# Optimization experiments

Hardware: AMD Instinct MI355X
Metric: run time of the kernel (lower is better)

## Reference

```python
import jax, jax.numpy as jnp
import numpy as np
from itertools import combinations

BASIS = 16  # identity + sums over every nonempty subset of the 4 set axes


def eq4_layer(x, coefs, bias):
    """Permutation-equivariant 4->4 set layer.
    x: (B, Din, n, n, n, n); coefs: (Din, Dout, 16); bias: (Dout,)
    Basis op 0 is identity; ops 1..15 are sums over each nonempty subset of the
    four set axes, broadcast back to full shape. We never stack the 16 full-size
    ops: pooled ops are contracted in their small (keepdims) form and broadcast-added.
    """
    out = jnp.einsum('ds,bdijkl->bsijkl', coefs[:, :, 0], x)
    b = 1
    for r in range(1, 5):
        for axes in combinations((2, 3, 4, 5), r):
            m = x.sum(axis=axes, keepdims=True)  # small marginal tensor
            out = out + jnp.einsum('ds,bd...->bs...', coefs[:, :, b], m)
            b += 1
    return out + bias.reshape(1, -1, 1, 1, 1, 1)


def setup_inputs() -> dict:
    key = jax.random.key(0)
    ks = jax.random.split(key, 9)
    B, n = 4, 24
    nembed, embed_dim, hid, out_dim = 1000, 15, 16, 16
    D = embed_dim + 1  # 16, = layers[0]
    s = 0.1
    return {
        'xcat': jax.random.randint(ks[0], (B, n), 0, nembed),
        'xfeat': jax.random.normal(ks[1], (B, n), dtype=jnp.float32),
        'embed': jax.random.normal(ks[2], (nembed, embed_dim), dtype=jnp.float32) * s,
        'coefs1': jax.random.normal(ks[3], (D, hid, BASIS), dtype=jnp.float32) * s,
        'bias1': jnp.zeros((hid,), dtype=jnp.float32),
        'coefs2': jax.random.normal(ks[4], (hid, out_dim, BASIS), dtype=jnp.float32) * s,
        'bias2': jnp.zeros((out_dim,), dtype=jnp.float32),
        'w_out': jax.random.normal(ks[5], (1, out_dim), dtype=jnp.float32) * s,
        'b_out': jnp.zeros((1,), dtype=jnp.float32),
    }


def reference(xcat, xfeat, embed, coefs1, bias1, coefs2, bias2, w_out, b_out):
    e = jax.nn.relu(embed[xcat])                       # (B, n, embed_dim)
    x = jnp.concatenate([e, xfeat[..., None]], axis=-1)  # (B, n, D)
    # 4th-order outer product per channel: (B, D, n, n, n, n)
    T = jnp.einsum('bid,bjd,bkd,bld->bdijkl', x, x, x, x)
    T = jax.nn.relu(eq4_layer(T, coefs1, bias1))
    T = jax.nn.relu(eq4_layer(T, coefs2, bias2))
    pooled = T.sum(axis=(2, 3, 4, 5))                  # (B, out_dim)
    return pooled @ w_out.T + b_out                    # (B, 1)
```

## Files before the change

### kernel.cpp

```cpp
#include <hip/hip_runtime.h>
#include <hip/hip_bf16.h>


#define NB 4
#define NN 24
#define ND 16
#define NS 16
#define NO 16
#define NKL 576

typedef unsigned int u32;
typedef unsigned short u16;

__device__ __forceinline__ u16 f2bf(float f) {
  u32 u = __float_as_uint(f);
  u = (u + 0x7fffu + ((u >> 16) & 1u)) >> 16;
  return (u16)u;
}
__device__ __forceinline__ float bflo(u32 u) { return __uint_as_float(u << 16); }
__device__ __forceinline__ float bfhi(u32 u) { return __uint_as_float(u & 0xffff0000u); }

__global__ __launch_bounds__(192, 2) void kb_eval(
    const int* __restrict__ xcat, const float* __restrict__ xfeat,
    const float* __restrict__ embed,
    const float* __restrict__ coefs1, const float* __restrict__ bias1,
    u32* __restrict__ T1g) {
  const int blk = blockIdx.x;
  const int j = blk % NN, i = (blk / NN) % NN, b = blk / (NN * NN);
  const int t = threadIdx.x;
  __shared__ float sx[NN * ND];
  __shared__ float SwL[16];
  __shared__ float Af[256], tb[256], tg[256], td[256];
  __shared__ float dconst[16];
  __shared__ __align__(16) float tabL[1152];

  for (int idx = t; idx < NN * ND; idx += 192) {
    int d = idx & 15, ii = idx >> 4;
    float v;
    if (d < 15) v = fmaxf(embed[xcat[b * NN + ii] * 15 + d], 0.f);
    else        v = xfeat[b * NN + ii];
    sx[idx] = v;
  }
  __syncthreads();
  if (t < 16) {
    float s = 0.f;
    for (int ii = 0; ii < NN; ++ii) s += sx[ii * 16 + t];
    SwL[t] = s;
  }
  __syncthreads();
  for (int idx = t; idx < 256; idx += 192) {
    int d = idx >> 4, s = idx & 15;
    const float* c = coefs1 + idx * 16;
    float xi = sx[i * 16 + d], xj = sx[j * 16 + d];
    float Sv = SwL[d];
    float S2 = Sv * Sv, S3 = S2 * Sv, S4 = S2 * S2, pij = xi * xj;
    Af[s * 16 + d] = c[0] * pij + c[1] * Sv * xj + c[2] * Sv * xi + c[5] * S2;
    tb[idx] = c[4] * Sv * pij + c[9] * S2 * xi + c[7] * S2 * xj + c[12] * S3;
    tg[idx] = c[3] * Sv * pij + c[8] * S2 * xi + c[6] * S2 * xj + c[11] * S3;
    td[idx] = c[10] * S2 * pij + c[14] * S3 * xi + c[13] * S3 * xj + c[15] * S4;
  }
  __syncthreads();
  if (t < 16) {
    float sd = 0.f;
    for (int d = 0; d < 16; ++d) sd += td[d * 16 + t];
    dconst[t] = sd + bias1[t];
  }
  __syncthreads();
  if (t < 128) {
    int s = t >> 3, m = t & 7;
    tabL[t] = __uint_as_float((u32)f2bf(Af[s * 16 + 2 * m]) |
                              ((u32)f2bf(Af[s * 16 + 2 * m + 1]) << 16));
  }
  for (int idx = t; idx < 768; idx += 192) {
    int pos = idx >> 4, s = idx & 15;
    if (pos < NN) {
      float acc = 0.f;
#pragma unroll
      for (int d = 0; d < 16; ++d) acc += tb[d * 16 + s] * sx[pos * 16 + d];
      tabL[128 + s * 32 + (pos % 8) * 4 + pos / 8] = acc;
    } else {
      int l = pos - NN;
      float acc = dconst[s];
#pragma unroll
      for (int d = 0; d < 16; ++d) acc += tg[d * 16 + s] * sx[l * 16 + d];
      tabL[640 + s * 32 + (l / 3) * 4 + l % 3] = acc;
    }
  }
  __syncthreads();

  const int l = t % NN, k0 = t / NN;
  const int lpos = (l / 3) * 4 + l % 3;
  float P0[16], P1[16], P2[16];
#pragma unroll
  for (int d = 0; d < 16; ++d) {
    float xl = sx[l * 16 + d];
    P0[d] = sx[k0 * 16 + d] * xl;
    P1[d] = sx[(k0 + 8) * 16 + d] * xl;
    P2[d] = sx[(k0 + 16) * 16 + d] * xl;
  }
  float pr0[16], pr1[16], pr2[16];
#pragma unroll
  for (int s = 0; s < 16; ++s) {
    const uint4* ap = (const uint4*)(tabL + s * 8);
    uint4 A0 = ap[0], A1 = ap[1];
    u32 qa[8] = {A0.x, A0.y, A0.z, A0.w, A1.x, A1.y, A1.z, A1.w};
    float Afr[16];
#pragma unroll
    for (int m = 0; m < 8; ++m) {
      Afr[2 * m] = bflo(qa[m]);
      Afr[2 * m + 1] = bfhi(qa[m]);
    }
    float4 vb4 = *(const float4*)(tabL + 128 + s * 32 + k0 * 4);
    float ct = tabL[640 + s * 32 + lpos];
    float v0 = vb4.x + ct, v1 = vb4.y + ct, v2 = vb4.z + ct;
#pragma unroll
    for (int d = 0; d < 16; ++d) {
      v0 += Afr[d] * P0[d];
      v1 += Afr[d] * P1[d];
      v2 += Afr[d] * P2[d];
    }
    pr0[s] = fmaxf(v0, 0.f);
    pr1[s] = fmaxf(v1, 0.f);
    pr2[s] = fmaxf(v2, 0.f);
  }
  auto emit = [&](float (&pr)[16], int kl) {
    u32 w[8];
#pragma unroll
    for (int m = 0; m < 8; ++m)
      w[m] = (u32)f2bf(pr[2 * m]) | ((u32)f2bf(pr[2 * m + 1]) << 16);
    uint4* gp = (uint4*)(T1g + ((size_t)blk * NKL + kl) * 8);
    gp[0] = make_uint4(w[0], w[1], w[2], w[3]);
    gp[1] = make_uint4(w[4], w[5], w[6], w[7]);
  };
  emit(pr0, t); emit(pr1, t + 192); emit(pr2, t + 384);
}

__global__ __launch_bounds__(256) void k3_marg(
    const u32* __restrict__ T1g, const float* __restrict__ coefs2,
    u32* __restrict__ mi_p, u32* __restrict__ mj_p,
    u32* __restrict__ mic_p, u32* __restrict__ mjc_p,
    float* __restrict__ quad_part) {
  const int t = threadIdx.x, bb = blockIdx.x;
  const int pos = bb * 256 + t;
  const bool isI = pos < 55296;
  const int p = isI ? pos : pos - 55296;
  __shared__ __align__(16) float ccT[16][20];
  __shared__ float qred[4][16];
  {
    int s = t >> 4, s2 = t & 15;
    ccT[s2][s] = coefs2[t * 16 + (isI ? 1 : 2)];
  }
  __syncthreads();
  const int ba = p / NKL, kl = p % NKL;
  const int b = ba / NN, a = ba % NN;
  const u32* base; size_t stride;
  if (isI) { base = T1g + ((size_t)(b * NN * NN + a) * NKL + kl) * 8; stride = (size_t)NN * NKL * 8; }
  else     { base = T1g + ((size_t)((b * NN + a) * NN) * NKL + kl) * 8; stride = (size_t)NKL * 8; }
  float raw[16];
#pragma unroll
  for (int s = 0; s < 16; ++s) raw[s] = 0.f;
#pragma unroll 4
  for (int c = 0; c < NN; ++c) {
    const uint4* q = (const uint4*)(base + c * stride);
    uint4 q0 = q[0], q1 = q[1];
    u32 qa[8] = {q0.x, q0.y, q0.z, q0.w, q1.x, q1.y, q1.z, q1.w};
#pragma unroll
    for (int m = 0; m < 8; ++m) {
      raw[2 * m] += bflo(qa[m]);
      raw[2 * m + 1] += bfhi(qa[m]);
    }
  }
  u32 rp[8], op[8];
#pragma unroll
  for (int m = 0; m < 8; ++m) {
    rp[m] = (u32)f2bf(raw[2 * m]) | ((u32)f2bf(raw[2 * m + 1]) << 16);
    float o0 = 0.f, o1 = 0.f;
#pragma unroll
    for (int w = 0; w < 4; ++w) {
      float4 m0 = ((const float4*)(&ccT[2 * m][0]))[w];
      float4 m1 = ((const float4*)(&ccT[2 * m + 1][0]))[w];
      o0 += m0.x * raw[4 * w] + m0.y * raw[4 * w + 1] + m0.z * raw[4 * w + 2] + m0.w * raw[4 * w + 3];
      o1 += m1.x * raw[4 * w] + m1.y * raw[4 * w + 1] + m1.z * raw[4 * w + 2] + m1.w * raw[4 * w + 3];
    }
    op[m] = (u32)f2bf(o0) | ((u32)f2bf(o1) << 16);
  }
  uint4* rdst = (uint4*)((isI ? mi_p : mj_p) + (size_t)p * 8);
  rdst[0] = make_uint4(rp[0], rp[1], rp[2], rp[3]);
  rdst[1] = make_uint4(rp[4], rp[5], rp[6], rp[7]);
  uint4* cdst = (uint4*)((isI ? mic_p : mjc_p) + (size_t)p * 8);
  cdst[0] = make_uint4(op[0], op[1], op[2], op[3]);
  cdst[1] = make_uint4(op[4], op[5], op[6], op[7]);
  if (isI) {
#pragma unroll
    for (int s = 0; s < 16; ++s) {
      float v = raw[s];
      for (int off = 32; off; off >>= 1) v += __shfl_xor(v, off, 64);
      raw[s] = v;
    }
    if ((t & 63) == 0) {
      int w = t >> 6;
#pragma unroll
      for (int s = 0; s < 16; ++s) qred[w][s] = raw[s];
    }
  }
  __syncthreads();
  if (isI && t < 16)
    quad_part[bb * 16 + t] = qred[0][t] + qred[1][t] + qred[2][t] + qred[3][t];
}

__global__ __launch_bounds__(256) void kd_derived(
    const u32* __restrict__ mi_p, const u32* __restrict__ mj_p,
    const float* __restrict__ quad_part, const float* __restrict__ coefs2,
    float* __restrict__ mijc, float* __restrict__ mikc, float* __restrict__ milc,
    float* __restrict__ mjkc, float* __restrict__ mjlc,
    float* __restrict__ mijkc, float* __restrict__ mijlc,
    float* __restrict__ miklc, float* __restrict__ mjklc,
    float* __restrict__ mijklc) {
  const int bb = blockIdx.x, t = threadIdx.x;
  __shared__ float cc[256];
  __shared__ float ex[32][17];
  __shared__ float tot[16];
  __shared__ float qr[64];
  if (bb < 360) {
    int tbl = bb / 72;
    cc[t] = coefs2[t * 16 + 5 + tbl];
    int pp = t >> 3, m = t & 7;
    int pos = (bb % 72) * 32 + pp;
    int b = pos / 576, rem = pos % 576;
    const u32* srcb; int stride;
    if (tbl == 0) { srcb = mi_p + ((size_t)b * 24 * 576 + rem) * 8 + m; stride = 576 * 8; }
    else if (tbl == 1) { int jj = rem / 24, l = rem % 24;
      srcb = mi_p + (((size_t)(b * 24 + jj)) * 576 + l) * 8 + m; stride = 24 * 8; }
    else if (tbl == 2) { int jj = rem / 24, k = rem % 24;
      srcb = mi_p + (((size_t)(b * 24 + jj)) * 576 + k * 24) * 8 + m; stride = 8; }
    else if (tbl == 3) { int ii = rem / 24, l = rem % 24;
      srcb = mj_p + (((size_t)(b * 24 + ii)) * 576 + l) * 8 + m; stride = 24 * 8; }
    else { int ii = rem / 24, k = rem % 24;
      srcb = mj_p + (((size_t)(b * 24 + ii)) * 576 + k * 24) * 8 + m; stride = 8; }
    float v0 = 0.f, v1 = 0.f;
#pragma unroll 4
    for (int x = 0; x < 24; ++x) {
      u32 u = srcb[(size_t)x * stride];
      v0 += bflo(u); v1 += bfhi(u);
    }
    ex[pp][2 * m] = v0;
    ex[pp][2 * m + 1] = v1;
    __syncthreads();
    float* dst = (tbl == 0 ? mijc : tbl == 1 ? mikc : tbl == 2 ? milc : tbl == 3 ? mjkc : mjlc);
    for (int idx = t; idx < 512; idx += 256) {
      int pp2 = idx >> 4, s2 = idx & 15;
      float o = 0.f;
#pragma unroll
      for (int ss = 0; ss < 16; ++ss) o += cc[ss * 16 + s2] * ex[pp2][ss];
      dst[(size_t)((bb % 72) * 32 + pp2) * 16 + s2] = o;
    }
    return;
  }
  if (bb < 360 + 384) {
    int idx = bb - 360;
    int tbl = idx / 96, rr = idx % 96;
    int b = rr / 24, a = rr % 24;
    cc[t] = coefs2[t * 16 + 11 + tbl];
    int gg = t >> 3, m = t & 7;
    const u32* src = (tbl == 3 ? mj_p : mi_p);
    float v0 = 0.f, v1 = 0.f;
#pragma unroll 2
    for (int it = 0; it < 18; ++it) {
      int u = gg + (it << 5);
      size_t addr;
      if (tbl == 0) { int j = u / 24, k = u % 24;
        addr = (((size_t)(b * 24 + j)) * 576 + k * 24 + a) * 8 + m; }
      else if (tbl == 1) { int j = u / 24, l = u % 24;
        addr = (((size_t)(b * 24 + j)) * 576 + a * 24 + l) * 8 + m; }
      else {
        addr = (((size_t)(b * 24 + a)) * 576 + u) * 8 + m; }
      u32 uu = src[addr];
      v0 += bflo(uu); v1 += bfhi(uu);
    }
    ex[gg][2 * m] = v0;
    ex[gg][2 * m + 1] = v1;
    __syncthreads();
    if (t < 16) {
      float w2 = 0.f;
#pragma unroll
      for (int g2 = 0; g2 < 32; ++g2) w2 += ex[g2][t];
      tot[t] = w2;
    }
    __syncthreads();
    if (t < 16) {
      float o = 0.f;
#pragma unroll
      for (int ss = 0; ss < 16; ++ss) o += cc[ss * 16 + t] * tot[ss];
      float* dst = (tbl == 0 ? mijkc : tbl == 1 ? mijlc : tbl == 2 ? miklc : mjklc);
      dst[(size_t)(b * 24 + a) * 16 + t] = o;
    }
    return;
  }
  if (t < 64) {
    int b = t >> 4, s = t & 15;
    float v = 0.f;
    for (int c = 0; c < 54; ++c) v += quad_part[(b * 54 + c) * 16 + s];
    qr[t] = v;
  }
  __syncthreads();
  if (t < 64) {
    int b = t >> 4, s2 = t & 15;
    float o = 0.f;
#pragma unroll
    for (int s = 0; s < 16; ++s) o += coefs2[(s * 16 + s2) * 16 + 15] * qr[b * 16 + s];
    mijklc[t] = o;
  }
}

__global__ __launch_bounds__(192, 2) void k5_final(
    const u32* __restrict__ T1g,
    const u32* __restrict__ mic_p, const u32* __restrict__ mjc_p,
    const float* __restrict__ mijc, const float* __restrict__ mikc,
    const float* __restrict__ milc, const float* __restrict__ mjkc,
    const float* __restrict__ mjlc,
    const float* __restrict__ mijkc, const float* __restrict__ mijlc,
    const float* __restrict__ miklc, const float* __restrict__ mjklc,
    const float* __restrict__ mijklc,
    const float* __restrict__ coefs2, const float* __restrict__ bias2,
    const float* __restrict__ w_out, float* __restrict__ pool_part) {
  const int orig = blockIdx.x;
  const int blk = (orig & 7) * 288 + (orig >> 3);
  const int j = blk % NN, i2 = (blk / NN) % NN, b = blk / (NN * NN);
  const int t = threadIdx.x;
  __shared__ __align__(16) u32 c2p[128];
  __shared__ __align__(16) float c2kT[16][20], c2lT[16][20], c2qT[16][20];
  __shared__ u32 T1p[NKL][9];
  __shared__ __align__(16) float rk[NN][20], rl[NN][20];
  __shared__ __align__(16) float rkl[16];
  __shared__ __align__(16) float Kt[NN][16], Lt[NN][16];
  __shared__ __align__(16) float cterm[16], wl[16];
  __shared__ float wsum[3];

  u32 qa0[8], qa1[8], qa2[8];
  auto loadT = [&](int c, u32 (&qa)[8]) {
    const int kl = t + 192 * c;
    const uint4* pt = (const uint4*)(T1g + ((size_t)blk * NKL + kl) * 8);
    uint4 t0 = pt[0], t1 = pt[1];
    qa[0] = t0.x; qa[1] = t0.y; qa[2] = t0.z; qa[3] = t0.w;
    qa[4] = t1.x; qa[5] = t1.y; qa[6] = t1.z; qa[7] = t1.w;
#pragma unroll
    for (int m = 0; m < 8; ++m) T1p[kl][m] = qa[m];
  };
  loadT(0, qa0); loadT(1, qa1); loadT(2, qa2);
  if (t < 128) {
    int s = t >> 3, m = t & 7;
    c2p[t] = (u32)f2bf(coefs2[(s * 16 + 2 * m) * 16]) |
             ((u32)f2bf(coefs2[(s * 16 + 2 * m + 1) * 16]) << 16);
  }
  for (int idx = t; idx < 256; idx += 192) {
    int s = idx >> 4, s2 = idx & 15;
    c2kT[s2][s] = coefs2[idx * 16 + 3];
    c2lT[s2][s] = coefs2[idx * 16 + 4];
    c2qT[s2][s] = coefs2[idx * 16 + 10];
  }
  __syncthreads();

  for (int idx = t; idx < NN * NS; idx += 192) {
    int a = idx >> 4, s = idx & 15, m = s >> 1;
    u32 odd = (u32)(s & 1);
    float sk = 0.f, sl = 0.f;
    for (int c = 0; c < NN; ++c) {
      u32 uk = T1p[c * NN + a][m];
      u32 ul = T1p[a * NN + c][m];
      sk += odd ? bfhi(uk) : bflo(uk);
      sl += odd ? bfhi(ul) : bflo(ul);
    }
    rk[a][s] = sk;
    rl[a][s] = sl;
  }
  __syncthreads();
  if (t < 16) {
    float v = 0.f;
    for (int a = 0; a < NN; ++a) v += rk[a][t];
    rkl[t] = v;
  }
  __syncthreads();
  for (int idx = t; idx < NN * NO; idx += 192) {
    int kk = idx >> 4, s2 = idx & 15;
    const float4* ck = (const float4*)(&c2kT[s2][0]);
    const float4* cl = (const float4*)(&c2lT[s2][0]);
    const float4* rkr = (const float4*)(&rk[kk][0]);
    const float4* rlr = (const float4*)(&rl[kk][0]);
    float ok = 0.f, ol = 0.f;
#pragma unroll
    for (int w = 0; w < 4; ++w) {
      float4 mk4 = ck[w], ml4 = cl[w], rk4 = rkr[w], rl4 = rlr[w];
      ok += mk4.x * rk4.x + mk4.y * rk4.y + mk4.z * rk4.z + mk4.w * rk4.w;
      ol += ml4.x * rl4.x + ml4.y * rl4.y + ml4.z * rl4.z + ml4.w * rl4.w;
    }
    Lt[kk][s2] = ok
               + mjkc[(size_t)((b * NN + i2) * NN + kk) * NS + s2]
               + mikc[(size_t)((b * NN + j) * NN + kk) * NS + s2]
               + mijkc[(size_t)(b * NN + kk) * NS + s2];
    Kt[kk][s2] = ol
               + mjlc[(size_t)((b * NN + i2) * NN + kk) * NS + s2]
               + milc[(size_t)((b * NN + j) * NN + kk) * NS + s2]
               + mijlc[(size_t)(b * NN + kk) * NS + s2];
  }
  if (t < NO) {
    float oq = 0.f;
#pragma unroll
    for (int s = 0; s < 16; ++s) oq += c2qT[t][s] * rkl[s];
    cterm[t] = oq
             + miklc[(size_t)(b * NN + j) * NS + t]
             + mjklc[(size_t)(b * NN + i2) * NS + t]
             + mijklc[(size_t)b * NS + t] + bias2[t];
    wl[t] = w_out[t];
  }
  __syncthreads();

  float acc0[16], acc1[16], acc2[16];
  auto initElem = [&](int c, u32 (&qa)[8], float (&acc)[16]) {
    const int kl = t + 192 * c;
    const int k = kl / NN, l = kl % NN;
    const uint4* pi = (const uint4*)(mic_p + ((size_t)((b * NN + j) * NKL + kl)) * 8);
    const uint4* pj = (const uint4*)(mjc_p + ((size_t)((b * NN + i2) * NKL + kl)) * 8);
    const float4* ps = (const float4*)(mijc + ((size_t)(b * NKL + kl)) * 16);
    uint4 i0 = pi[0], i1 = pi[1];
    uint4 j0 = pj[0], j1 = pj[1];
    float4 s0 = ps[0], s1 = ps[1], s2v = ps[2], s3 = ps[3];
    u32 ia[8] = {i0.x, i0.y, i0.z, i0.w, i1.x, i1.y, i1.z, i1.w};
    u32 ja[8] = {j0.x, j0.y, j0.z, j0.w, j1.x, j1.y, j1.z, j1.w};
    float sv[16];
    ((float4*)sv)[0] = s0; ((float4*)sv)[1] = s1; ((float4*)sv)[2] = s2v; ((float4*)sv)[3] = s3;
#pragma unroll
    for (int m = 0; m < 8; ++m) {
      acc[2 * m]     = cterm[2 * m]     + Kt[k][2 * m]     + Lt[l][2 * m]
                     + bflo(ia[m]) + bflo(ja[m]) + sv[2 * m];
      acc[2 * m + 1] = cterm[2 * m + 1] + Kt[k][2 * m + 1] + Lt[l][2 * m + 1]
                     + bfhi(ia[m]) + bfhi(ja[m]) + sv[2 * m + 1];
    }
  };
  initElem(0, qa0, acc0); initElem(1, qa1, acc1); initElem(2, qa2, acc2);

#pragma unroll
  for (int s = 0; s < 16; ++s) {
    const uint4* cp = (const uint4*)(c2p + s * 8);
    uint4 C0 = cp[0], C1 = cp[1];
    u32 ca[8] = {C0.x, C0.y, C0.z, C0.w, C1.x, C1.y, C1.z, C1.w};
    float row[16];
#pragma unroll
    for (int m = 0; m < 8; ++m) {
      row[2 * m] = bflo(ca[m]);
      row[2 * m + 1] = bfhi(ca[m]);
    }
    float v0 = (s & 1) ? bfhi(qa0[s >> 1]) : bflo(qa0[s >> 1]);
    float v1 = (s & 1) ? bfhi(qa1[s >> 1]) : bflo(qa1[s >> 1]);
    float v2 = (s & 1) ? bfhi(qa2[s >> 1]) : bflo(qa2[s >> 1]);
#pragma unroll
    for (int s2 = 0; s2 < 16; ++s2) {
      acc0[s2] += row[s2] * v0;
      acc1[s2] += row[s2] * v1;
      acc2[s2] += row[s2] * v2;
    }
  }
  float p = 0.f;
#pragma unroll
  for (int s2 = 0; s2 < 16; ++s2)
    p += wl[s2] * (fmaxf(acc0[s2], 0.f) + fmaxf(acc1[s2], 0.f) + fmaxf(acc2[s2], 0.f));
  for (int off = 32; off; off >>= 1) p += __shfl_down(p, off, 64);
  if ((t & 63) == 0) wsum[t >> 6] = p;
  __syncthreads();
  if (t == 0) pool_part[blk] = wsum[0] + wsum[1] + wsum[2];
}

__global__ __launch_bounds__(256) void k6_out(
    const float* __restrict__ pool_part, const float* __restrict__ b_out,
    float* __restrict__ out) {
  const int t = threadIdx.x;
  const int b = t >> 6, lane = t & 63;
  float v = 0.f;
  for (int c = lane; c < 576; c += 64) v += pool_part[b * 576 + c];
  for (int off = 32; off; off >>= 1) v += __shfl_down(v, off, 64);
  if (lane == 0) out[b] = v + b_out[0];
}

extern "C" void kernel_launch(void* const* d_in, const int* in_sizes, int n_in,
                              void* d_out, int out_size, void* d_ws, size_t ws_size,
                              hipStream_t stream) {
  (void)in_sizes; (void)n_in; (void)out_size; (void)ws_size;
  const int*   xcat   = (const int*)d_in[0];
  const float* xfeat  = (const float*)d_in[1];
  const float* embed  = (const float*)d_in[2];
  const float* coefs1 = (const float*)d_in[3];
  const float* bias1  = (const float*)d_in[4];
  const float* coefs2 = (const float*)d_in[5];
  const float* bias2  = (const float*)d_in[6];
  const float* w_out  = (const float*)d_in[7];
  const float* b_out  = (const float*)d_in[8];
  float* out = (float*)d_out;
  char* ws = (char*)d_ws;

  u32*   T1g      = (u32*)(ws + 0);
  u32*   mi_p     = (u32*)(ws + 42467328);
  u32*   mj_p     = (u32*)(ws + 44236800);
  u32*   mic_p    = (u32*)(ws + 46006272);
  u32*   mjc_p    = (u32*)(ws + 47775744);
  float* mijc     = (float*)(ws + 49545216);
  float* mikc     = (float*)(ws + 49692672);
  float* milc     = (float*)(ws + 49840128);
  float* mjkc     = (float*)(ws + 49987584);
  float* mjlc     = (float*)(ws + 50135040);
  float* mijkc    = (float*)(ws + 50282496);
  float* mijlc    = (float*)(ws + 50288640);
  float* miklc    = (float*)(ws + 50294784);
  float* mjklc    = (float*)(ws + 50300928);
  float* mijklc   = (float*)(ws + 50307072);
  float* quad_part= (float*)(ws + 50307328);
  float* pool_part= (float*)(ws + 50321152);

  kb_eval<<<NB * NN * NN, 192, 0, stream>>>(xcat, xfeat, embed, coefs1, bias1, T1g);
  k3_marg<<<432, 256, 0, stream>>>(T1g, coefs2, mi_p, mj_p, mic_p, mjc_p, quad_part);
  kd_derived<<<745, 256, 0, stream>>>(mi_p, mj_p, quad_part, coefs2,
                                      mijc, mikc, milc, mjkc, mjlc,
                                      mijkc, mijlc, miklc, mjklc, mijklc);
  k5_final<<<NB * NN * NN, 192, 0, stream>>>(T1g, mic_p, mjc_p,
                                             mijc, mikc, milc, mjkc, mjlc,
                                             mijkc, mijlc, miklc, mjklc, mijklc,
                                             coefs2, bias2, w_out, pool_part);
  k6_out<<<1, 256, 0, stream>>>(pool_part, b_out, out);
}
```

Baseline: 98.84 us.

## Store first-layer intermediate tensor as per-tile scaled FP8 instead of bf16

The first-layer output T1, the largest intermediate, is now quantized to FP8 with one scale per (b,i,j) tile, chosen from a block-wide max reduction. This halves the bytes written by kb_eval and read by k3_marg and k5_final, and shrinks the shared-memory staging in k5_final. In exchange it adds a reduction and barrier in kb_eval, per-element scale multiplies and FP8 decode in the consumers, and much coarser precision (3-bit mantissa), which may exceed accuracy tolerance.

```diff
diff --git a/kernel.cpp b/kernel.cpp
--- a/kernel.cpp
+++ b/kernel.cpp
@@ -11,6 +11,7 @@
 
 typedef unsigned int u32;
 typedef unsigned short u16;
+typedef float f32x2 __attribute__((ext_vector_type(2)));
 
 __device__ __forceinline__ u16 f2bf(float f) {
   u32 u = __float_as_uint(f);
@@ -19,12 +20,20 @@
 }
 __device__ __forceinline__ float bflo(u32 u) { return __uint_as_float(u << 16); }
 __device__ __forceinline__ float bfhi(u32 u) { return __uint_as_float(u & 0xffff0000u); }
+__device__ __forceinline__ f32x2 dec2(u32 w) {
+  return __builtin_amdgcn_cvt_pk_f32_fp8((int)w, false);
+}
+__device__ __forceinline__ u32 enc4(float a, float b, float c, float d) {
+  u32 w = (u32)__builtin_amdgcn_cvt_pk_fp8_f32(a, b, 0, false);
+  w = (u32)__builtin_amdgcn_cvt_pk_fp8_f32(c, d, (int)w, true);
+  return w;
+}
 
 __global__ __launch_bounds__(192, 2) void kb_eval(
     const int* __restrict__ xcat, const float* __restrict__ xfeat,
     const float* __restrict__ embed,
     const float* __restrict__ coefs1, const float* __restrict__ bias1,
-    u32* __restrict__ T1g) {
+    u32* __restrict__ T1g, float* __restrict__ scale_g) {
   const int blk = blockIdx.x;
   const int j = blk % NN, i = (blk / NN) % NN, b = blk / (NN * NN);
   const int t = threadIdx.x;
@@ -33,6 +42,7 @@
   __shared__ float Af[256], tb[256], tg[256], td[256];
   __shared__ float dconst[16];
   __shared__ __align__(16) float tabL[1152];
+  __shared__ float redm[3];
 
   for (int idx = t; idx < NN * ND; idx += 192) {
     int d = idx & 15, ii = idx >> 4;
@@ -123,20 +133,33 @@
     pr1[s] = fmaxf(v1, 0.f);
     pr2[s] = fmaxf(v2, 0.f);
   }
+  float tmax = 0.f;
+#pragma unroll
+  for (int s = 0; s < 16; ++s)
+    tmax = fmaxf(tmax, fmaxf(pr0[s], fmaxf(pr1[s], pr2[s])));
+  for (int off = 32; off; off >>= 1) tmax = fmaxf(tmax, __shfl_xor(tmax, off, 64));
+  if ((t & 63) == 0) redm[t >> 6] = tmax;
+  __syncthreads();
+  float tilemax = fmaxf(redm[0], fmaxf(redm[1], redm[2]));
+  float scale, scinv;
+  if (tilemax > 1e-30f) { scale = 440.f / tilemax; scinv = tilemax / 440.f; }
+  else                  { scale = 0.f; scinv = 0.f; }
+  if (t == 0) scale_g[blk] = scinv;
+
   auto emit = [&](float (&pr)[16], int kl) {
-    u32 w[8];
-#pragma unroll
-    for (int m = 0; m < 8; ++m)
-      w[m] = (u32)f2bf(pr[2 * m]) | ((u32)f2bf(pr[2 * m + 1]) << 16);
-    uint4* gp = (uint4*)(T1g + ((size_t)blk * NKL + kl) * 8);
-    gp[0] = make_uint4(w[0], w[1], w[2], w[3]);
-    gp[1] = make_uint4(w[4], w[5], w[6], w[7]);
+    u32 w[4];
+#pragma unroll
+    for (int m = 0; m < 4; ++m)
+      w[m] = enc4(pr[4 * m] * scale, pr[4 * m + 1] * scale,
+                  pr[4 * m + 2] * scale, pr[4 * m + 3] * scale);
+    *(uint4*)(T1g + ((size_t)blk * NKL + kl) * 4) = make_uint4(w[0], w[1], w[2], w[3]);
   };
   emit(pr0, t); emit(pr1, t + 192); emit(pr2, t + 384);
 }
 
 __global__ __launch_bounds__(256) void k3_marg(
-    const u32* __restrict__ T1g, const float* __restrict__ coefs2,
+    const u32* __restrict__ T1g, const float* __restrict__ scale_g,
+    const float* __restrict__ coefs2,
     u32* __restrict__ mi_p, u32* __restrict__ mj_p,
     u32* __restrict__ mic_p, u32* __restrict__ mjc_p,
     float* __restrict__ quad_part) {
@@ -154,20 +177,25 @@
   const int ba = p / NKL, kl = p % NKL;
   const int b = ba / NN, a = ba % NN;
   const u32* base; size_t stride;
-  if (isI) { base = T1g + ((size_t)(b * NN * NN + a) * NKL + kl) * 8; stride = (size_t)NN * NKL * 8; }
-  else     { base = T1g + ((size_t)((b * NN + a) * NN) * NKL + kl) * 8; stride = (size_t)NKL * 8; }
+  if (isI) { base = T1g + ((size_t)(b * NN * NN + a) * NKL + kl) * 4; stride = (size_t)NN * NKL * 4; }
+  else     { base = T1g + ((size_t)((b * NN + a) * NN) * NKL + kl) * 4; stride = (size_t)NKL * 4; }
   float raw[16];
 #pragma unroll
   for (int s = 0; s < 16; ++s) raw[s] = 0.f;
 #pragma unroll 4
   for (int c = 0; c < NN; ++c) {
-    const uint4* q = (const uint4*)(base + c * stride);
-    uint4 q0 = q[0], q1 = q[1];
-    u32 qa[8] = {q0.x, q0.y, q0.z, q0.w, q1.x, q1.y, q1.z, q1.w};
-#pragma unroll
-    for (int m = 0; m < 8; ++m) {
-      raw[2 * m] += bflo(qa[m]);
-      raw[2 * m + 1] += bfhi(qa[m]);
+    const uint4 q = *(const uint4*)(base + c * stride);
+    const int tile = isI ? ((b * NN + c) * NN + a) : ((b * NN + a) * NN + c);
+    const float sc = scale_g[tile];
+    u32 qa[4] = {q.x, q.y, q.z, q.w};
+#pragma unroll
+    for (int m = 0; m < 4; ++m) {
+      f32x2 d0 = dec2(qa[m]);
+      f32x2 d1 = dec2(qa[m] >> 16);
+      raw[4 * m]     += sc * d0.x;
+      raw[4 * m + 1] += sc * d0.y;
+      raw[4 * m + 2] += sc * d1.x;
+      raw[4 * m + 3] += sc * d1.y;
     }
   }
   u32 rp[8], op[8];
@@ -313,7 +341,7 @@
 }
 
 __global__ __launch_bounds__(192, 2) void k5_final(
-    const u32* __restrict__ T1g,
+    const u32* __restrict__ T1g, const float* __restrict__ scale_g,
     const u32* __restrict__ mic_p, const u32* __restrict__ mjc_p,
     const float* __restrict__ mijc, const float* __restrict__ mikc,
     const float* __restrict__ milc, const float* __restrict__ mjkc,
@@ -329,22 +357,21 @@
   const int t = threadIdx.x;
   __shared__ __align__(16) u32 c2p[128];
   __shared__ __align__(16) float c2kT[16][20], c2lT[16][20], c2qT[16][20];
-  __shared__ u32 T1p[NKL][9];
+  __shared__ u32 T1p[NKL][5];
   __shared__ __align__(16) float rk[NN][20], rl[NN][20];
   __shared__ __align__(16) float rkl[16];
   __shared__ __align__(16) float Kt[NN][16], Lt[NN][16];
   __shared__ __align__(16) float cterm[16], wl[16];
   __shared__ float wsum[3];
 
-  u32 qa0[8], qa1[8], qa2[8];
-  auto loadT = [&](int c, u32 (&qa)[8]) {
+  const float sc = scale_g[blk];
+  u32 qa0[4], qa1[4], qa2[4];
+  auto loadT = [&](int c, u32 (&qa)[4]) {
     const int kl = t + 192 * c;
-    const uint4* pt = (const uint4*)(T1g + ((size_t)blk * NKL + kl) * 8);
-    uint4 t0 = pt[0], t1 = pt[1];
-    qa[0] = t0.x; qa[1] = t0.y; qa[2] = t0.z; qa[3] = t0.w;
-    qa[4] = t1.x; qa[5] = t1.y; qa[6] = t1.z; qa[7] = t1.w;
-#pragma unroll
-    for (int m = 0; m < 8; ++m) T1p[kl][m] = qa[m];
+    const uint4 q = *(const uint4*)(T1g + ((size_t)blk * NKL + kl) * 4);
+    qa[0] = q.x; qa[1] = q.y; qa[2] = q.z; qa[3] = q.w;
+#pragma unroll
+    for (int m = 0; m < 4; ++m) T1p[kl][m] = qa[m];
   };
   loadT(0, qa0); loadT(1, qa1); loadT(2, qa2);
   if (t < 128) {
@@ -360,18 +387,18 @@
   }
   __syncthreads();
 
-  for (int idx = t; idx < NN * NS; idx += 192) {
-    int a = idx >> 4, s = idx & 15, m = s >> 1;
-    u32 odd = (u32)(s & 1);
-    float sk = 0.f, sl = 0.f;
+  {
+    int a = t >> 3, pr_ = t & 7, wIdx = pr_ >> 1;
+    int sh = (pr_ & 1) * 16;
+    float s0k = 0.f, s1k = 0.f, s0l = 0.f, s1l = 0.f;
     for (int c = 0; c < NN; ++c) {
-      u32 uk = T1p[c * NN + a][m];
-      u32 ul = T1p[a * NN + c][m];
-      sk += odd ? bfhi(uk) : bflo(uk);
-      sl += odd ? bfhi(ul) : bflo(ul);
-    }
-    rk[a][s] = sk;
-    rl[a][s] = sl;
+      f32x2 dk = dec2(T1p[c * NN + a][wIdx] >> sh);
+      f32x2 dl = dec2(T1p[a * NN + c][wIdx] >> sh);
+      s0k += dk.x; s1k += dk.y;
+      s0l += dl.x; s1l += dl.y;
+    }
+    rk[a][2 * pr_] = sc * s0k; rk[a][2 * pr_ + 1] = sc * s1k;
+    rl[a][2 * pr_] = sc * s0l; rl[a][2 * pr_ + 1] = sc * s1l;
   }
   __syncthreads();
   if (t < 16) {
@@ -415,7 +442,7 @@
   __syncthreads();
 
   float acc0[16], acc1[16], acc2[16];
-  auto initElem = [&](int c, u32 (&qa)[8], float (&acc)[16]) {
+  auto initElem = [&](int c, float (&acc)[16]) {
     const int kl = t + 192 * c;
     const int k = kl / NN, l = kl % NN;
     const uint4* pi = (const uint4*)(mic_p + ((size_t)((b * NN + j) * NKL + kl)) * 8);
@@ -436,7 +463,7 @@
                      + bfhi(ia[m]) + bfhi(ja[m]) + sv[2 * m + 1];
     }
   };
-  initElem(0, qa0, acc0); initElem(1, qa1, acc1); initElem(2, qa2, acc2);
+  initElem(0, acc0); initElem(1, acc1); initElem(2, acc2);
 
 #pragma unroll
   for (int s = 0; s < 16; ++s) {
@@ -449,9 +476,12 @@
       row[2 * m] = bflo(ca[m]);
       row[2 * m + 1] = bfhi(ca[m]);
     }
-    float v0 = (s & 1) ? bfhi(qa0[s >> 1]) : bflo(qa0[s >> 1]);
-    float v1 = (s & 1) ? bfhi(qa1[s >> 1]) : bflo(qa1[s >> 1]);
-    float v2 = (s & 1) ? bfhi(qa2[s >> 1]) : bflo(qa2[s >> 1]);
+    f32x2 d0 = dec2(qa0[s >> 2] >> (((s >> 1) & 1) * 16));
+    f32x2 d1 = dec2(qa1[s >> 2] >> (((s >> 1) & 1) * 16));
+    f32x2 d2 = dec2(qa2[s >> 2] >> (((s >> 1) & 1) * 16));
+    float v0 = ((s & 1) ? d0.y : d0.x) * sc;
+    float v1 = ((s & 1) ? d1.y : d1.x) * sc;
+    float v2 = ((s & 1) ? d2.y : d2.x) * sc;
 #pragma unroll
     for (int s2 = 0; s2 < 16; ++s2) {
       acc0[s2] += row[s2] * v0;
@@ -497,29 +527,32 @@
   char* ws = (char*)d_ws;
 
   u32*   T1g      = (u32*)(ws + 0);
-  u32*   mi_p     = (u32*)(ws + 42467328);
-  u32*   mj_p     = (u32*)(ws + 44236800);
-  u32*   mic_p    = (u32*)(ws + 46006272);
-  u32*   mjc_p    = (u32*)(ws + 47775744);
-  float* mijc     = (float*)(ws + 49545216);
-  float* mikc     = (float*)(ws + 49692672);
-  float* milc     = (float*)(ws + 49840128);
-  float* mjkc     = (float*)(ws + 49987584);
-  float* mjlc     = (float*)(ws + 50135040);
-  float* mijkc    = (float*)(ws + 50282496);
-  float* mijlc    = (float*)(ws + 50288640);
-  float* miklc    = (float*)(ws + 50294784);
-  float* mjklc    = (float*)(ws + 50300928);
-  float* mijklc   = (float*)(ws + 50307072);
-  float* quad_part= (float*)(ws + 50307328);
-  float* pool_part= (float*)(ws + 50321152);
-
-  kb_eval<<<NB * NN * NN, 192, 0, stream>>>(xcat, xfeat, embed, coefs1, bias1, T1g);
-  k3_marg<<<432, 256, 0, stream>>>(T1g, coefs2, mi_p, mj_p, mic_p, mjc_p, quad_part);
+  float* scale_g  = (float*)(ws + 21233664);
+  u32*   mi_p     = (u32*)(ws + 21242880);
+  u32*   mj_p     = (u32*)(ws + 23012352);
+  u32*   mic_p    = (u32*)(ws + 24781824);
+  u32*   mjc_p    = (u32*)(ws + 26551296);
+  float* mijc     = (float*)(ws + 28320768);
+  float* mikc     = (float*)(ws + 28468224);
+  float* milc     = (float*)(ws + 28615680);
+  float* mjkc     = (float*)(ws + 28763136);
+  float* mjlc     = (float*)(ws + 28910592);
+  float* mijkc    = (float*)(ws + 29058048);
+  float* mijlc    = (float*)(ws + 29064192);
+  float* miklc    = (float*)(ws + 29070336);
+  float* mjklc    = (float*)(ws + 29076480);
+  float* mijklc   = (float*)(ws + 29082624);
+  float* quad_part= (float*)(ws + 29082880);
+  float* pool_part= (float*)(ws + 29096704);
+
+  kb_eval<<<NB * NN * NN, 192, 0, stream>>>(xcat, xfeat, embed, coefs1, bias1,
+                                            T1g, scale_g);
+  k3_marg<<<432, 256, 0, stream>>>(T1g, scale_g, coefs2, mi_p, mj_p, mic_p,
+                                   mjc_p, quad_part);
   kd_derived<<<745, 256, 0, stream>>>(mi_p, mj_p, quad_part, coefs2,
                                       mijc, mikc, milc, mjkc, mjlc,
                                       mijkc, mijlc, miklc, mjklc, mijklc);
-  k5_final<<<NB * NN * NN, 192, 0, stream>>>(T1g, mic_p, mjc_p,
+  k5_final<<<NB * NN * NN, 192, 0, stream>>>(T1g, scale_g, mic_p, mjc_p,
                                              mijc, mikc, milc, mjkc, mjlc,
                                              mijkc, mijlc, miklc, mjklc, mijklc,
                                              coefs2, bias2, w_out, pool_part);
```

Measured after the change: 88.67 us. -10.3%, faster.
